# Kernel tuning notes

Measured on AMD Instinct MI355X. Metric: run time of the kernel, lower is better.

Reference implementation:

```python
import jax, jax.numpy as jnp
import numpy as np

V, E, H = 50257, 256, 256
B, S = 64, 2048


def setup_inputs() -> dict:
    key = jax.random.key(0)
    ks = jax.random.split(key, 24)
    u = (1.0 / H) ** 0.5
    def U(k, shape):
        return jax.random.uniform(k, shape, jnp.float32, -u, u)
    inp = {
        "inputs": jax.random.randint(ks[0], (B, S), 0, V, dtype=jnp.int32),
        "h0": jax.random.normal(ks[1], (1, B, H), jnp.float32),
        "c0": jax.random.normal(ks[2], (1, B, H), jnp.float32),
        "emb": jax.random.normal(ks[3], (V, E), jnp.float32) * 0.02,
    }
    for i, n in enumerate(["w_ii", "w_if", "w_ig", "w_io"]):
        inp[n] = U(ks[4 + i], (H, E))
    for i, n in enumerate(["w_hi", "w_hf", "w_hg", "w_ho"]):
        inp[n] = U(ks[8 + i], (H, H))
    for i, n in enumerate(["b_ii", "b_if", "b_ig", "b_io", "b_hi", "b_hf", "b_hg", "b_ho"]):
        inp[n] = U(ks[12 + i], (H,))
    return inp


def _lstm(x, h0, c0, w_ii, w_if, w_ig, w_io, w_hi, w_hf, w_hg, w_ho,
          b_ii, b_if, b_ig, b_io, b_hi, b_hf, b_hg, b_ho):
    # x: (B, S, E). Precompute all input projections (batched GEMMs) once.
    xi = jnp.einsum('bse,he->bsh', x, w_ii) + b_ii + b_hi  # (B,S,H)
    xf = jnp.einsum('bse,he->bsh', x, w_if) + b_if + b_hf
    xg = jnp.einsum('bse,he->bsh', x, w_ig) + b_ig + b_hg
    xo = jnp.einsum('bse,he->bsh', x, w_io) + b_io + b_ho
    # move time to leading axis for scan: (S,B,H)
    xs = (xi.transpose(1, 0, 2), xf.transpose(1, 0, 2),
          xg.transpose(1, 0, 2), xo.transpose(1, 0, 2))

    def step(carry, ts):
        h, c = carry  # (B,H)
        xi_t, xf_t, xg_t, xo_t = ts
        i_t = jax.nn.sigmoid(xi_t + h @ w_hi.T)
        f_t = jax.nn.sigmoid(xf_t + h @ w_hf.T)
        g_t = jnp.tanh(xg_t + h @ w_hg.T)
        o_t = jax.nn.sigmoid(xo_t + h @ w_ho.T)
        c_new = f_t * c + i_t * g_t
        h_new = o_t * jnp.tanh(c_new)
        return (h_new, c_new), h_new

    (h_f, c_f), out = jax.lax.scan(step, (h0[0], c0[0]), xs)  # out: (S,B,H)
    return out.transpose(1, 0, 2), h_f[None], c_f[None]


def reference(inputs, h0, c0, emb, w_ii, w_if, w_ig, w_io, w_hi, w_hf, w_hg, w_ho,
              b_ii, b_if, b_ig, b_io, b_hi, b_hf, b_hg, b_ho):
    # nn.Embedding(padding_idx=0): row 0 is zero and receives no gradient
    emb_z = emb.at[0].set(0.0)
    x = emb_z[inputs]  # (B,S,E)
    return _lstm(x, h0, c0, w_ii, w_if, w_ig, w_io, w_hi, w_hf, w_hg, w_ho,
                 b_ii, b_if, b_ig, b_io, b_hi, b_hf, b_hg, b_ho)
```

## Files before the change

### kernel.cpp

```cpp
#include <hip/hip_runtime.h>
#include <hip/hip_fp16.h>
#include <cstdint>
#include <cstddef>

#define B_ 64
#define S_ 2048
#define H_ 256
#define E_ 256
#define NG 1024

typedef __attribute__((ext_vector_type(8))) short short8v;
typedef __attribute__((ext_vector_type(4))) float float4v;
typedef __fp16 half2v __attribute__((ext_vector_type(2)));

__device__ __forceinline__ short f2bf(float f) {
  uint32_t u = __float_as_uint(f);
  u = (u + 0x7fffu + ((u >> 16) & 1u)) >> 16;
  return (short)u;
}
__device__ __forceinline__ float sigf(float x) { return 1.f / (1.f + __expf(-x)); }
__device__ __forceinline__ float tanhf_fast(float x) {
  float ax = fabsf(x);
  float e = __expf(-2.f * ax);
  float t = (1.f - e) / (1.f + e);
  return copysignf(t, x);
}
__device__ __forceinline__ uint32_t pkh2(float a, float b) {
  return __builtin_bit_cast(uint32_t, __floats2half2_rn(a, b));
}

__device__ __forceinline__ float dot2f(uint32_t w, uint32_t h, float acc) {
#if __has_builtin(__builtin_amdgcn_fdot2)
  return __builtin_amdgcn_fdot2(__builtin_bit_cast(half2v, w),
                                __builtin_bit_cast(half2v, h), acc, false);
#else
  __half2 hw = __builtin_bit_cast(__half2, w);
  __half2 hh = __builtin_bit_cast(__half2, h);
  acc = fmaf(__half2float(hw.x), __half2float(hh.x), acc);
  acc = fmaf(__half2float(hw.y), __half2float(hh.y), acc);
  return acc;
#endif
}

__device__ __forceinline__ float red_q4(float x) {
  x += __builtin_bit_cast(float, __builtin_amdgcn_update_dpp(
           0, __builtin_bit_cast(int, x), 0x128, 0xf, 0xf, true));
  float a = x, b = x;
  asm("v_permlane32_swap_b32 %0, %1" : "+v"(a), "+v"(b));
  return a + b;
}

__global__ __launch_bounds__(256, 2)
void lstm_xproj(const int* __restrict__ idx, const float* __restrict__ emb,
                const float* __restrict__ w0, const float* __restrict__ w1,
                const float* __restrict__ w2, const float* __restrict__ w3,
                const float* __restrict__ bi0, const float* __restrict__ bi1,
                const float* __restrict__ bi2, const float* __restrict__ bi3,
                const float* __restrict__ bh0, const float* __restrict__ bh1,
                const float* __restrict__ bh2, const float* __restrict__ bh3,
                __half* __restrict__ pre, int s0, int Cc) {
  __shared__ __align__(16) short Ak[4][128][8];
  __shared__ __align__(16) short Bk[4][128][8];
  __shared__ int ridx[128];

  const int tid = threadIdx.x;
  const int bm = blockIdx.x, bn = blockIdx.y;
  const int n0 = bn * 128;
  const int g = bn >> 1;
  const int ng = (bn & 1) * 128;
  const float* wp  = (g == 0) ? w0  : (g == 1) ? w1  : (g == 2) ? w2  : w3;
  const float* bip = (g == 0) ? bi0 : (g == 1) ? bi1 : (g == 2) ? bi2 : bi3;
  const float* bhp = (g == 0) ? bh0 : (g == 1) ? bh1 : (g == 2) ? bh2 : bh3;

  if (tid < 128) {
    int m = bm * 128 + tid;
    int bb = m / Cc;
    int ss = m - bb * Cc;
    ridx[tid] = idx[bb * S_ + s0 + ss];
  }

  float4v z = {0.f, 0.f, 0.f, 0.f};
  float4v acc[4][4];
#pragma unroll
  for (int mi = 0; mi < 4; ++mi)
#pragma unroll
    for (int ni = 0; ni < 4; ++ni) acc[mi][ni] = z;

  const int wv = tid >> 6, lane = tid & 63;
  const int wr = wv >> 1, wc = wv & 1;
  const int lr = lane & 15, ks = lane >> 4;
  const int sr = tid >> 3, seg = tid & 7;

  for (int kt = 0; kt < 8; ++kt) {
    const int k0 = kt * 32;
    __syncthreads();
#pragma unroll
    for (int it = 0; it < 4; ++it) {
      int r = sr + it * 32;
      int tok = ridx[r];
      float4 va = make_float4(0.f, 0.f, 0.f, 0.f);
      if (tok != 0) va = *(const float4*)(emb + (size_t)tok * E_ + k0 + seg * 4);
      short4 sa; sa.x = f2bf(va.x); sa.y = f2bf(va.y); sa.z = f2bf(va.z); sa.w = f2bf(va.w);
      *(short4*)&Ak[seg >> 1][r][(seg & 1) * 4] = sa;
      float4 vb = *(const float4*)(wp + (size_t)(ng + r) * E_ + k0 + seg * 4);
      short4 sb; sb.x = f2bf(vb.x); sb.y = f2bf(vb.y); sb.z = f2bf(vb.z); sb.w = f2bf(vb.w);
      *(short4*)&Bk[seg >> 1][r][(seg & 1) * 4] = sb;
    }
    __syncthreads();
    short8v af[4], bfv[4];
#pragma unroll
    for (int mi = 0; mi < 4; ++mi) af[mi] = *(short8v*)&Ak[ks][wr * 64 + mi * 16 + lr][0];
#pragma unroll
    for (int ni = 0; ni < 4; ++ni) bfv[ni] = *(short8v*)&Bk[ks][wc * 64 + ni * 16 + lr][0];
#pragma unroll
    for (int mi = 0; mi < 4; ++mi)
#pragma unroll
      for (int ni = 0; ni < 4; ++ni)
        acc[mi][ni] = __builtin_amdgcn_mfma_f32_16x16x32_bf16(af[mi], bfv[ni], acc[mi][ni], 0, 0, 0);
  }

#pragma unroll
  for (int ni = 0; ni < 4; ++ni) {
    int jj = ng + wc * 64 + ni * 16 + lr;
    float bias = bip[jj] + bhp[jj];
    int jglob = n0 + wc * 64 + ni * 16 + lr;
#pragma unroll
    for (int mi = 0; mi < 4; ++mi) {
#pragma unroll
      for (int rr = 0; rr < 4; ++rr) {
        int m = bm * 128 + wr * 64 + mi * 16 + (lane >> 4) * 4 + rr;
        pre[(size_t)m * NG + jglob] = __float2half(acc[mi][ni][rr] + bias);
      }
    }
  }
}

__global__ __launch_bounds__(512, 2)
void lstm_rec(const __half* __restrict__ pre,
              const float* wh_i, const float* wh_f,
              const float* wh_g, const float* wh_o,
              const float* __restrict__ h0, const float* __restrict__ c0,
              float* out, float* cstate,
              int s0, int Cc) {
  __shared__ uint32_t wlds32[256 * 128];
  __shared__ uint32_t hshp[144];

  const int b = blockIdx.x;
  const int t = threadIdx.x;
  const int lane = t & 63, wave = t >> 6;
  const int q4 = ((lane >> 3) & 1) | ((lane >> 5) << 1);
  const int jp = (wave << 4) | (((lane >> 4) & 1) << 3) | (lane & 7);
  const int j0 = 2 * jp;
  const bool fin = ((lane & 40) == 0);
  const int sw = (jp & 7) << 2;

#pragma unroll 8
  for (int i = 0; i < 64; ++i) {
    int idx2 = t + 512 * i;
    int row = idx2 >> 7, col = idx2 & 127;
    float2 v = *(const float2*)(wh_o + 2 * idx2);
    wlds32[row * 128 + (col ^ (((row >> 1) & 7) << 2))] = pkh2(v.x, v.y);
  }

  uint32_t wI0[32], wI1[32], wF0[32], wF1[32], wG0[32], wG1[32];
  {
    const float4* pI0 = (const float4*)(wh_i + (size_t)j0 * 256 + q4 * 64);
    const float4* pI1 = (const float4*)(wh_i + (size_t)(j0 + 1) * 256 + q4 * 64);
    const float4* pF0 = (const float4*)(wh_f + (size_t)j0 * 256 + q4 * 64);
    const float4* pF1 = (const float4*)(wh_f + (size_t)(j0 + 1) * 256 + q4 * 64);
    const float4* pG0 = (const float4*)(wh_g + (size_t)j0 * 256 + q4 * 64);
    const float4* pG1 = (const float4*)(wh_g + (size_t)(j0 + 1) * 256 + q4 * 64);
#pragma unroll
    for (int k = 0; k < 16; ++k) {
      float4 v;
      v = pI0[k]; wI0[2 * k] = pkh2(v.x, v.y); wI0[2 * k + 1] = pkh2(v.z, v.w);
      v = pI1[k]; wI1[2 * k] = pkh2(v.x, v.y); wI1[2 * k + 1] = pkh2(v.z, v.w);
      v = pF0[k]; wF0[2 * k] = pkh2(v.x, v.y); wF0[2 * k + 1] = pkh2(v.z, v.w);
      v = pF1[k]; wF1[2 * k] = pkh2(v.x, v.y); wF1[2 * k + 1] = pkh2(v.z, v.w);
      v = pG0[k]; wG0[2 * k] = pkh2(v.x, v.y); wG0[2 * k + 1] = pkh2(v.z, v.w);
      v = pG1[k]; wG1[2 * k] = pkh2(v.x, v.y); wG1[2 * k + 1] = pkh2(v.z, v.w);
    }
  }

  if (t < 128) {
    float2 hp = (s0 == 0) ? *(const float2*)(h0 + b * H_ + 2 * t)
                          : *(const float2*)(cstate + b * 512 + 256 + 2 * t);
    hshp[(t >> 5) * 36 + (t & 31)] = pkh2(hp.x, hp.y);
  }
  float cR0 = 0.f, cR1 = 0.f, hN0 = 0.f, hN1 = 0.f;
  if (fin) {
    float2 cv = (s0 == 0) ? *(const float2*)(c0 + b * H_ + j0)
                          : *(const float2*)(cstate + b * 512 + j0);
    cR0 = cv.x; cR1 = cv.y;
  }
  __syncthreads();

  const __half2* pbase = (const __half2*)(pre + (size_t)b * (size_t)Cc * NG);
  const uint32_t* wrow0 = wlds32 + (size_t)j0 * 128 + q4 * 32;
  const uint32_t* wrow1 = wrow0 + 128;
  const uint32_t* hq = hshp + q4 * 36;

#define HV_(c8)  (*(const uint4*)(hq + (c8) * 4))
#define WO0_(c8) (*(const uint4*)(wrow0 + (((c8) * 4) ^ sw)))
#define WO1_(c8) (*(const uint4*)(wrow1 + (((c8) * 4) ^ sw)))
#define CONS_(c8, hv, wa, wb)                                   \
  aO0 = dot2f(wa.x, hv.x, aO0); aO0 = dot2f(wa.y, hv.y, aO0);   \
  aO0 = dot2f(wa.z, hv.z, aO0); aO0 = dot2f(wa.w, hv.w, aO0);   \
  aO1 = dot2f(wb.x, hv.x, aO1); aO1 = dot2f(wb.y, hv.y, aO1);   \
  aO1 = dot2f(wb.z, hv.z, aO1); aO1 = dot2f(wb.w, hv.w, aO1);   \
  aI0 = dot2f(wI0[(c8) * 4 + 0], hv.x, aI0);                    \
  aI0 = dot2f(wI0[(c8) * 4 + 1], hv.y, aI0);                    \
  aI0 = dot2f(wI0[(c8) * 4 + 2], hv.z, aI0);                    \
  aI0 = dot2f(wI0[(c8) * 4 + 3], hv.w, aI0);                    \
  aI1 = dot2f(wI1[(c8) * 4 + 0], hv.x, aI1);                    \
  aI1 = dot2f(wI1[(c8) * 4 + 1], hv.y, aI1);                    \
  aI1 = dot2f(wI1[(c8) * 4 + 2], hv.z, aI1);                    \
  aI1 = dot2f(wI1[(c8) * 4 + 3], hv.w, aI1);                    \
  aF0 = dot2f(wF0[(c8) * 4 + 0], hv.x, aF0);                    \
  aF0 = dot2f(wF0[(c8) * 4 + 1], hv.y, aF0);                    \
  aF0 = dot2f(wF0[(c8) * 4 + 2], hv.z, aF0);                    \
  aF0 = dot2f(wF0[(c8) * 4 + 3], hv.w, aF0);                    \
  aF1 = dot2f(wF1[(c8) * 4 + 0], hv.x, aF1);                    \
  aF1 = dot2f(wF1[(c8) * 4 + 1], hv.y, aF1);                    \
  aF1 = dot2f(wF1[(c8) * 4 + 2], hv.z, aF1);                    \
  aF1 = dot2f(wF1[(c8) * 4 + 3], hv.w, aF1);                    \
  aG0 = dot2f(wG0[(c8) * 4 + 0], hv.x, aG0);                    \
  aG0 = dot2f(wG0[(c8) * 4 + 1], hv.y, aG0);                    \
  aG0 = dot2f(wG0[(c8) * 4 + 2], hv.z, aG0);                    \
  aG0 = dot2f(wG0[(c8) * 4 + 3], hv.w, aG0);                    \
  aG1 = dot2f(wG1[(c8) * 4 + 0], hv.x, aG1);                    \
  aG1 = dot2f(wG1[(c8) * 4 + 1], hv.y, aG1);                    \
  aG1 = dot2f(wG1[(c8) * 4 + 2], hv.z, aG1);                    \
  aG1 = dot2f(wG1[(c8) * 4 + 3], hv.w, aG1);

  for (int tl = 0; tl < Cc; ++tl) {
    float2 pI = {0.f, 0.f}, pF = {0.f, 0.f}, pG = {0.f, 0.f}, pO = {0.f, 0.f};
    if (fin) {
      const __half2* pp = pbase + (size_t)tl * 512;
      pI = __half22float2(pp[jp]);
      pF = __half22float2(pp[128 + jp]);
      pG = __half22float2(pp[256 + jp]);
      pO = __half22float2(pp[384 + jp]);
    }

    float aI0 = 0.f, aI1 = 0.f, aF0 = 0.f, aF1 = 0.f;
    float aG0 = 0.f, aG1 = 0.f, aO0 = 0.f, aO1 = 0.f;
    {
      uint4 hvA = HV_(0), waA = WO0_(0), wbA = WO1_(0);
      uint4 hvB = HV_(1), waB = WO0_(1), wbB = WO1_(1);
      CONS_(0, hvA, waA, wbA);
      hvA = HV_(2); waA = WO0_(2); wbA = WO1_(2);
      CONS_(1, hvB, waB, wbB);
      hvB = HV_(3); waB = WO0_(3); wbB = WO1_(3);
      CONS_(2, hvA, waA, wbA);
      hvA = HV_(4); waA = WO0_(4); wbA = WO1_(4);
      CONS_(3, hvB, waB, wbB);
      hvB = HV_(5); waB = WO0_(5); wbB = WO1_(5);
      CONS_(4, hvA, waA, wbA);
      hvA = HV_(6); waA = WO0_(6); wbA = WO1_(6);
      CONS_(5, hvB, waB, wbB);
      hvB = HV_(7); waB = WO0_(7); wbB = WO1_(7);
      CONS_(6, hvA, waA, wbA);
      CONS_(7, hvB, waB, wbB);
    }

    aI0 = red_q4(aI0); aI1 = red_q4(aI1);
    aF0 = red_q4(aF0); aF1 = red_q4(aF1);
    aG0 = red_q4(aG0); aG1 = red_q4(aG1);
    aO0 = red_q4(aO0); aO1 = red_q4(aO1);
    __syncthreads();

    if (fin) {
      float xi0 = aI0 + pI.x, xi1 = aI1 + pI.y;
      float xf0 = aF0 + pF.x, xf1 = aF1 + pF.y;
      float xg0 = aG0 + pG.x, xg1 = aG1 + pG.y;
      float xo0 = aO0 + pO.x, xo1 = aO1 + pO.y;
      cR0 = sigf(xf0) * cR0 + sigf(xi0) * tanhf_fast(xg0);
      cR1 = sigf(xf1) * cR1 + sigf(xi1) * tanhf_fast(xg1);
      hN0 = sigf(xo0) * tanhf_fast(cR0);
      hN1 = sigf(xo1) * tanhf_fast(cR1);
      *(float2*)(out + ((size_t)b * S_ + (s0 + tl)) * H_ + j0) = make_float2(hN0, hN1);
      hshp[(jp >> 5) * 36 + (jp & 31)] = pkh2(hN0, hN1);
    }
    __syncthreads();
  }
#undef CONS_
#undef WO1_
#undef WO0_
#undef HV_

  if (fin) {
    *(float2*)(cstate + b * 512 + j0) = make_float2(cR0, cR1);
    *(float2*)(cstate + b * 512 + 256 + j0) = make_float2(hN0, hN1);
    if (s0 + Cc == S_) {
      float* hfp = out + (size_t)B_ * S_ * H_;
      float* cfp = hfp + (size_t)B_ * H_;
      *(float2*)(hfp + b * H_ + j0) = make_float2(hN0, hN1);
      *(float2*)(cfp + b * H_ + j0) = make_float2(cR0, cR1);
    }
  }
}

extern "C" void kernel_launch(void* const* d_in, const int* in_sizes, int n_in,
                              void* d_out, int out_size, void* d_ws, size_t ws_size,
                              hipStream_t stream) {
  (void)in_sizes; (void)n_in; (void)out_size;
  const int* idx = (const int*)d_in[0];
  const float* h0 = (const float*)d_in[1];
  const float* c0 = (const float*)d_in[2];
  const float* emb = (const float*)d_in[3];
  const float* w_ii = (const float*)d_in[4];
  const float* w_if = (const float*)d_in[5];
  const float* w_ig = (const float*)d_in[6];
  const float* w_io = (const float*)d_in[7];
  const float* w_hi = (const float*)d_in[8];
  const float* w_hf = (const float*)d_in[9];
  const float* w_hg = (const float*)d_in[10];
  const float* w_ho = (const float*)d_in[11];
  const float* b_ii = (const float*)d_in[12];
  const float* b_if = (const float*)d_in[13];
  const float* b_ig = (const float*)d_in[14];
  const float* b_io = (const float*)d_in[15];
  const float* b_hi = (const float*)d_in[16];
  const float* b_hf = (const float*)d_in[17];
  const float* b_hg = (const float*)d_in[18];
  const float* b_ho = (const float*)d_in[19];
  float* out = (float*)d_out;

  char* ws = (char*)d_ws;
  float* cstate = (float*)ws;
  __half* pre = (__half*)(ws + 131072);
  size_t avail = (ws_size > 131072) ? ws_size - 131072 : 0;
  long long cmax = (long long)(avail / ((size_t)B_ * NG * sizeof(__half)));
  int C = (int)((cmax > S_) ? S_ : cmax);
  C &= ~1;
  if (C < 2) C = 2;

  for (int s0 = 0; s0 < S_; s0 += C) {
    int Cc = (S_ - s0 < C) ? (S_ - s0) : C;
    dim3 gg((unsigned)((64 * Cc) / 128), 8);
    lstm_xproj<<<gg, 256, 0, stream>>>(idx, emb, w_ii, w_if, w_ig, w_io,
                                       b_ii, b_if, b_ig, b_io,
                                       b_hi, b_hf, b_hg, b_ho, pre, s0, Cc);
    lstm_rec<<<64, 512, 0, stream>>>(pre, w_hi, w_hf, w_hg, w_ho, h0, c0,
                                     out, cstate, s0, Cc);
  }
}
```

Before: 5.148 ms.

## Double-buffer LDS hidden state to drop one barrier per recurrent step

The hidden-state LDS buffer is doubled, so each step reads one half and writes the other. That cuts the per-timestep barriers from two to one. The precomputed input-gate values for the next step are now loaded in the middle of the current step's dot products, hiding global load latency. The first W_o LDS fragments for the next iteration are also loaded at the end of each iteration. Together these shorten the serial critical path of the recurrence, at the cost of a few more registers and twice the hidden-state LDS.

```diff
diff --git a/kernel.cpp b/kernel.cpp
--- a/kernel.cpp
+++ b/kernel.cpp
@@ -143,7 +143,7 @@
               float* out, float* cstate,
               int s0, int Cc) {
   __shared__ uint32_t wlds32[256 * 128];
-  __shared__ uint32_t hshp[144];
+  __shared__ uint32_t hshp[288];
 
   const int b = blockIdx.x;
   const int t = threadIdx.x;
@@ -195,10 +195,12 @@
   }
   __syncthreads();
 
-  const __half2* pbase = (const __half2*)(pre + (size_t)b * (size_t)Cc * NG);
+  const uint32_t* pb32 = (const uint32_t*)(pre + (size_t)b * (size_t)Cc * NG);
   const uint32_t* wrow0 = wlds32 + (size_t)j0 * 128 + q4 * 32;
   const uint32_t* wrow1 = wrow0 + 128;
-  const uint32_t* hq = hshp + q4 * 36;
+  const uint32_t* hq0 = hshp + q4 * 36;
+  uint32_t* hw0 = hshp + (jp >> 5) * 36 + (jp & 31);
+  uint32_t* hw1 = hw0 + 144;
 
 #define HV_(c8)  (*(const uint4*)(hq + (c8) * 4))
 #define WO0_(c8) (*(const uint4*)(wrow0 + (((c8) * 4) ^ sw)))
@@ -233,44 +235,49 @@
   aG1 = dot2f(wG1[(c8) * 4 + 2], hv.z, aG1);                    \
   aG1 = dot2f(wG1[(c8) * 4 + 3], hv.w, aG1);
 
+  uint4 waA = WO0_(0), wbA = WO1_(0);
+  uint4 waB = WO0_(1), wbB = WO1_(1);
+  uint32_t pC0 = 0, pC1 = 0, pC2 = 0, pC3 = 0;
+  if (fin) {
+    pC0 = pb32[jp];       pC1 = pb32[128 + jp];
+    pC2 = pb32[256 + jp]; pC3 = pb32[384 + jp];
+  }
+
   for (int tl = 0; tl < Cc; ++tl) {
-    float2 pI = {0.f, 0.f}, pF = {0.f, 0.f}, pG = {0.f, 0.f}, pO = {0.f, 0.f};
-    if (fin) {
-      const __half2* pp = pbase + (size_t)tl * 512;
-      pI = __half22float2(pp[jp]);
-      pF = __half22float2(pp[128 + jp]);
-      pG = __half22float2(pp[256 + jp]);
-      pO = __half22float2(pp[384 + jp]);
-    }
+    __syncthreads();
+    const uint32_t* hq = hq0 + ((tl & 1) ? 144 : 0);
+    uint4 hvA = HV_(0), hvB = HV_(1);
 
     float aI0 = 0.f, aI1 = 0.f, aF0 = 0.f, aF1 = 0.f;
     float aG0 = 0.f, aG1 = 0.f, aO0 = 0.f, aO1 = 0.f;
-    {
-      uint4 hvA = HV_(0), waA = WO0_(0), wbA = WO1_(0);
-      uint4 hvB = HV_(1), waB = WO0_(1), wbB = WO1_(1);
-      CONS_(0, hvA, waA, wbA);
-      hvA = HV_(2); waA = WO0_(2); wbA = WO1_(2);
-      CONS_(1, hvB, waB, wbB);
-      hvB = HV_(3); waB = WO0_(3); wbB = WO1_(3);
-      CONS_(2, hvA, waA, wbA);
-      hvA = HV_(4); waA = WO0_(4); wbA = WO1_(4);
-      CONS_(3, hvB, waB, wbB);
-      hvB = HV_(5); waB = WO0_(5); wbB = WO1_(5);
-      CONS_(4, hvA, waA, wbA);
-      hvA = HV_(6); waA = WO0_(6); wbA = WO1_(6);
-      CONS_(5, hvB, waB, wbB);
-      hvB = HV_(7); waB = WO0_(7); wbB = WO1_(7);
-      CONS_(6, hvA, waA, wbA);
-      CONS_(7, hvB, waB, wbB);
-    }
+
+    CONS_(0, hvA, waA, wbA); waA = WO0_(2); wbA = WO1_(2); hvA = HV_(2);
+    CONS_(1, hvB, waB, wbB); waB = WO0_(3); wbB = WO1_(3); hvB = HV_(3);
+
+    uint32_t pN0 = pC0, pN1 = pC1, pN2 = pC2, pN3 = pC3;
+    if (fin && (tl + 1 < Cc)) {
+      const uint32_t* pp = pb32 + (size_t)(tl + 1) * 512;
+      pN0 = pp[jp];       pN1 = pp[128 + jp];
+      pN2 = pp[256 + jp]; pN3 = pp[384 + jp];
+    }
+
+    CONS_(2, hvA, waA, wbA); waA = WO0_(4); wbA = WO1_(4); hvA = HV_(4);
+    CONS_(3, hvB, waB, wbB); waB = WO0_(5); wbB = WO1_(5); hvB = HV_(5);
+    CONS_(4, hvA, waA, wbA); waA = WO0_(6); wbA = WO1_(6); hvA = HV_(6);
+    CONS_(5, hvB, waB, wbB); waB = WO0_(7); wbB = WO1_(7); hvB = HV_(7);
+    CONS_(6, hvA, waA, wbA); waA = WO0_(0); wbA = WO1_(0);
+    CONS_(7, hvB, waB, wbB); waB = WO0_(1); wbB = WO1_(1);
 
     aI0 = red_q4(aI0); aI1 = red_q4(aI1);
     aF0 = red_q4(aF0); aF1 = red_q4(aF1);
     aG0 = red_q4(aG0); aG1 = red_q4(aG1);
     aO0 = red_q4(aO0); aO1 = red_q4(aO1);
-    __syncthreads();
 
     if (fin) {
+      float2 pI = __half22float2(__builtin_bit_cast(__half2, pC0));
+      float2 pF = __half22float2(__builtin_bit_cast(__half2, pC1));
+      float2 pG = __half22float2(__builtin_bit_cast(__half2, pC2));
+      float2 pO = __half22float2(__builtin_bit_cast(__half2, pC3));
       float xi0 = aI0 + pI.x, xi1 = aI1 + pI.y;
       float xf0 = aF0 + pF.x, xf1 = aF1 + pF.y;
       float xg0 = aG0 + pG.x, xg1 = aG1 + pG.y;
@@ -280,9 +287,9 @@
       hN0 = sigf(xo0) * tanhf_fast(cR0);
       hN1 = sigf(xo1) * tanhf_fast(cR1);
       *(float2*)(out + ((size_t)b * S_ + (s0 + tl)) * H_ + j0) = make_float2(hN0, hN1);
-      hshp[(jp >> 5) * 36 + (jp & 31)] = pkh2(hN0, hN1);
-    }
-    __syncthreads();
+      *((tl & 1) ? hw0 : hw1) = pkh2(hN0, hN1);
+    }
+    pC0 = pN0; pC1 = pN1; pC2 = pN2; pC3 = pN3;
   }
 #undef CONS_
 #undef WO1_
```

Result: slower. 7.331 ms (+42.4%).
